# Kernel optimization log

Hardware: AMD Instinct MI355X
Metric: run time of the kernel (lower is better)

The kernel has to match this reference:

```python
import jax, jax.numpy as jnp
import numpy as np

N_STATE = 256   # complex state size n (real state is 2n)
N_IN = 128
BATCH = 16
T_STEPS = 2048
H_STEP = 0.01
EPS = 1e-3
LAM_RE_MIN, LAM_RE_MAX, MAX_PHASE = -5.0, -0.5, 6.283


def setup_inputs() -> dict:
    rng = np.random.default_rng(0)
    n, nu = N_STATE, N_IN
    # trainable params (as in torch __init__)
    u1 = rng.random(n)
    u2 = rng.random(n) * 2.0 - 1.0
    alpha = np.log(-(u1 * (LAM_RE_MAX - LAM_RE_MIN) + LAM_RE_MIN)).astype(np.float32)
    theta = (MAX_PHASE * u2).astype(np.float32)
    B_re = (rng.standard_normal((n, nu)) / np.sqrt(2.0 * nu)).astype(np.float32)
    B_im = (rng.standard_normal((n, nu)) / np.sqrt(2.0 * nu)).astype(np.float32)
    # fixed basis-change buffers: rho (normalized), T_inv, P = rho @ T_inv, Pinv
    H1 = rng.standard_normal((n, n))
    H2 = rng.standard_normal((n, n))
    rho = np.block([[H1, -H2], [H2, H1]])
    rho = rho / np.linalg.norm(rho)
    I = np.eye(n)
    T_inv = (1.0 / np.sqrt(2.0)) * np.block([[I, I], [-1j * I, 1j * I]])
    P = rho.astype(np.complex128) @ T_inv
    Pinv = np.linalg.inv(P)
    key = jax.random.key(0)
    k1, k2 = jax.random.split(key)
    return {
        "xi_init": jax.random.normal(k1, (BATCH, 1, 2 * n), dtype=jnp.float32),
        "u_log": jax.random.normal(k2, (BATCH, T_STEPS, nu), dtype=jnp.float32),
        "alpha": jnp.asarray(alpha),
        "theta": jnp.asarray(theta),
        "B_re": jnp.asarray(B_re),
        "B_im": jnp.asarray(B_im),
        "P_re": jnp.asarray(P.real, dtype=jnp.float32),
        "P_im": jnp.asarray(P.imag, dtype=jnp.float32),
        "Pinv_re": jnp.asarray(Pinv.real, dtype=jnp.float32),
        "Pinv_im": jnp.asarray(Pinv.imag, dtype=jnp.float32),
        "T": T_STEPS,
    }


def reference(xi_init, u_log, alpha, theta, B_re, B_im, P_re, P_im, Pinv_re, Pinv_im, T):
    n = alpha.shape[0]
    lam = (-jnp.exp(alpha) - EPS) + 1j * theta          # (n,) complex64
    Bc = B_re + 1j * B_im                               # (n, nu)
    P = P_re + 1j * P_im                                # (2n, 2n)
    Pinv = Pinv_re + 1j * Pinv_im                       # (2n, 2n)
    xi0 = xi_init[:, 0, :]                              # (B, 2n) real

    def step(xi, u_t):
        # xi: (B, 2n) real state; u_t: (B, nu)
        x_tilde = xi.astype(jnp.complex64) @ Pinv.T     # (B, 2n) complex
        x_bar = x_tilde[:, :n]                          # (B, n)
        x_bar_dot = lam * x_bar + u_t.astype(jnp.complex64) @ Bc.T
        x_tilde_dot = jnp.concatenate([x_bar_dot, jnp.conj(x_bar_dot)], axis=-1)
        x_dot = (x_tilde_dot @ P.T).real                # (B, 2n)
        xi_new = xi + H_STEP * x_dot
        return xi_new, xi_new

    u_seq = jnp.swapaxes(u_log, 0, 1)                   # (T, B, nu)
    _, xs = jax.lax.scan(step, xi0, u_seq)              # (T, B, 2n)
    # torch _sim logs xi_init, then skips xi after t=0, logs xi after t=1..T-1
    x_log = jnp.concatenate([xi0[None], xs[1:]], axis=0)  # (T, B, 2n)
    return jnp.swapaxes(x_log, 0, 1)                    # (B, T, 2n)
```

## Files before the change

kernel.cpp:

```cpp
#include <hip/hip_runtime.h>
#include <hip/hip_bf16.h>
#include <cstddef>
#include <cstdint>

#define N_ST 256
#define TWO_N 512
#define NU 128
#define BATCH 16
#define TSTEPS 2048
#define MTOT (BATCH * TSTEPS)
#define H_STEP 0.01f
#define EPS_V 0.001f
#define NCHUNK 32
#define CHUNKL 64

typedef __attribute__((ext_vector_type(4))) float f32x4;
typedef __attribute__((ext_vector_type(4))) short s16x4;
typedef __attribute__((ext_vector_type(8))) short s16x8;

#define OFF_FPK    0
#define OFF_ZPK    8388608
#define OFF_UPK    16777216
#define OFF_WT     18874368
#define OFF_WF     19005440
#define OFF_D      19038208
#define OFF_XBAR0  19039232
#define OFF_E      19047424
#define OFF_CINIT  19309568

static __device__ __forceinline__ float bf2f(short s) {
    return __uint_as_float(((unsigned)(unsigned short)s) << 16);
}

__global__ __launch_bounds__(256) void prep_all(
    const float* __restrict__ P_re, const float* __restrict__ P_im,
    const float* __restrict__ B_re, const float* __restrict__ B_im,
    const float* __restrict__ alpha, const float* __restrict__ theta,
    short* __restrict__ Wtpk, short* __restrict__ Wfpk,
    float* __restrict__ dbuf)
{
    int blk = blockIdx.x, tid = threadIdx.x;
    if (blk < 1024) {
        int idx = blk * 256 + tid;
        int j = idx >> 9, c = idx & 511;
        float v;
        if (c < N_ST) v = P_re[j * TWO_N + c] + P_re[j * TWO_N + c + N_ST];
        else          v = P_im[j * TWO_N + c] - P_im[j * TWO_N + c - N_ST];
        __hip_bfloat16 b = __float2bfloat16(v);
        Wtpk[((size_t)(j >> 4) * TWO_N + c) * 16 + (j & 15)] = *(short*)&b;
    } else if (blk < 1280) {
        int idx = (blk - 1024) * 256 + tid;
        int k = idx >> 9, c = idx & 511;
        float v = (c < N_ST) ? B_re[c * NU + k] : B_im[(c - N_ST) * NU + k];
        __hip_bfloat16 b = __float2bfloat16(H_STEP * v);
        Wfpk[((size_t)(c >> 4) * NU + k) * 16 + (c & 15)] = *(short*)&b;
    } else {
        int i = tid;
        float dr = 1.0f + H_STEP * (-expf(alpha[i]) - EPS_V);
        float di = H_STEP * theta[i];
        float pr = 1.0f, pi = 0.0f;
        for (int k = 0; k < CHUNKL; ++k) { float nr = pr * dr - pi * di; pi = pr * di + pi * dr; pr = nr; }
        dbuf[i] = dr; dbuf[N_ST + i] = di; dbuf[2 * N_ST + i] = pr; dbuf[3 * N_ST + i] = pi;
    }
}

__global__ __launch_bounds__(256) void xbar0_kernel(
    const float* __restrict__ Pinv_re, const float* __restrict__ Pinv_im,
    const float* __restrict__ xi0, float* __restrict__ xbar0)
{
    __shared__ float xs[BATCH * TWO_N];
    int tid = threadIdx.x;
#pragma unroll
    for (int q = 0; q < 8; ++q)
        *reinterpret_cast<float4*>(&xs[(q * 256 + tid) * 4]) =
            *reinterpret_cast<const float4*>(&xi0[(q * 256 + tid) * 4]);
    __syncthreads();

    int wv = tid >> 6, l = tid & 63;
    int i = blockIdx.x * 4 + wv;
    float rp[BATCH] = {}, ip[BATCH] = {};
#pragma unroll
    for (int q = 0; q < 8; ++q) {
        int j = q * 64 + l;
        float pr = Pinv_re[(size_t)i * TWO_N + j];
        float pi = Pinv_im[(size_t)i * TWO_N + j];
#pragma unroll
        for (int b = 0; b < BATCH; ++b) {
            float x = xs[b * TWO_N + j];
            rp[b] = fmaf(pr, x, rp[b]);
            ip[b] = fmaf(pi, x, ip[b]);
        }
    }
#pragma unroll
    for (int m = 1; m < 64; m <<= 1) {
#pragma unroll
        for (int b = 0; b < BATCH; ++b) {
            rp[b] += __shfl_xor(rp[b], m, 64);
            ip[b] += __shfl_xor(ip[b], m, 64);
        }
    }
    if (l == 0) {
#pragma unroll
        for (int b = 0; b < BATCH; ++b) {
            xbar0[b * TWO_N + i] = rp[b];
            xbar0[b * TWO_N + N_ST + i] = ip[b];
        }
    }
}

__global__ __launch_bounds__(256) void upack(const float* __restrict__ u, short* __restrict__ upk) {
    __shared__ short st[64 * 132];
    int tid = threadIdx.x, bid = blockIdx.x;
    const float* up = u + (size_t)bid * 8192;
#pragma unroll
    for (int q = 0; q < 8; ++q) {
        int idx = q * 1024 + tid * 4;
        float4 v = *reinterpret_cast<const float4*>(up + idx);
        int m = idx >> 7, k = idx & 127;
        s16x4 pv;
        __hip_bfloat16 b0 = __float2bfloat16(v.x); pv[0] = *(short*)&b0;
        __hip_bfloat16 b1 = __float2bfloat16(v.y); pv[1] = *(short*)&b1;
        __hip_bfloat16 b2 = __float2bfloat16(v.z); pv[2] = *(short*)&b2;
        __hip_bfloat16 b3 = __float2bfloat16(v.w); pv[3] = *(short*)&b3;
        *reinterpret_cast<__shared__ s16x4*>(&st[m * 132 + k]) = pv;
    }
    __syncthreads();
    short* op = upk + (size_t)bid * 8192;
#pragma unroll
    for (int q2 = 0; q2 < 4; ++q2) {
        int o = q2 * 2048 + tid * 8;
        int ml = o & 15, k = (o >> 4) & 127, sl = o >> 11;
        s16x8 w;
#pragma unroll
        for (int r = 0; r < 8; ++r) w[r] = st[(sl * 16 + ml + r) * 132 + k];
        *reinterpret_cast<s16x8*>(op + o) = w;
    }
}

template <int K, bool PACKOUT>
__global__ __launch_bounds__(256, 2) void gemm_mfma(const short* __restrict__ Apk,
                                                    const short* __restrict__ Bpk,
                                                    float* __restrict__ Cf,
                                                    short* __restrict__ Cp,
                                                    const float* __restrict__ xi0) {
    __shared__ __align__(1024) short lds[16384];
    const int tid = threadIdx.x;
    const int wid = tid >> 6, lane = tid & 63;
    const int m0 = blockIdx.x * 128, n0 = blockIdx.y * 128;
    const int wm = wid >> 1, wn = wid & 1;
    f32x4 acc[4][4] = {};
    const size_t slabStride = (size_t)K * 16;
    const unsigned ldsBase = (unsigned)(uintptr_t)(__attribute__((address_space(3))) short*)&lds[0];

#define STAGE(buf, kk)                                                                              \
    do {                                                                                            \
        const short* gA0 = Apk + ((size_t)(m0 >> 4) + wid)     * slabStride + (size_t)(kk) * 16 + lane * 8; \
        const short* gA1 = Apk + ((size_t)(m0 >> 4) + wid + 4) * slabStride + (size_t)(kk) * 16 + lane * 8; \
        const short* gB0 = Bpk + ((size_t)(n0 >> 4) + wid)     * slabStride + (size_t)(kk) * 16 + lane * 8; \
        const short* gB1 = Bpk + ((size_t)(n0 >> 4) + wid + 4) * slabStride + (size_t)(kk) * 16 + lane * 8; \
        __builtin_amdgcn_global_load_lds((const __attribute__((address_space(1))) void*)gA0,        \
            (__attribute__((address_space(3))) void*)&lds[(buf) * 4096 + wid * 512], 16, 0, 0);     \
        __builtin_amdgcn_global_load_lds((const __attribute__((address_space(1))) void*)gA1,        \
            (__attribute__((address_space(3))) void*)&lds[(buf) * 4096 + (wid + 4) * 512], 16, 0, 0); \
        __builtin_amdgcn_global_load_lds((const __attribute__((address_space(1))) void*)gB0,        \
            (__attribute__((address_space(3))) void*)&lds[8192 + (buf) * 4096 + wid * 512], 16, 0, 0); \
        __builtin_amdgcn_global_load_lds((const __attribute__((address_space(1))) void*)gB1,        \
            (__attribute__((address_space(3))) void*)&lds[8192 + (buf) * 4096 + (wid + 4) * 512], 16, 0, 0); \
    } while (0)

    STAGE(0, 0);
    asm volatile("s_waitcnt vmcnt(0)" ::: "memory");
    __syncthreads();
    int cur = 0;
    for (int kk = 0; kk < K; kk += 32) {
        if (kk + 32 < K) STAGE(cur ^ 1, kk + 32);

        s16x4 al[4], ah[4], bl[4], bh[4];
        const unsigned aB = ldsBase + (unsigned)cur * 8192;
        const unsigned bB = ldsBase + 16384u + (unsigned)cur * 8192;
#pragma unroll
        for (int t = 0; t < 4; ++t) {
            unsigned ad = aB + ((unsigned)(wm * 4 + t) << 10) + ((unsigned)lane << 3);
            unsigned bd = bB + ((unsigned)(wn * 4 + t) << 10) + ((unsigned)lane << 3);
            asm volatile("ds_read_b64_tr_b16 %0, %1 offset:0"   : "=v"(al[t]) : "v"(ad));
            asm volatile("ds_read_b64_tr_b16 %0, %1 offset:512" : "=v"(ah[t]) : "v"(ad));
            asm volatile("ds_read_b64_tr_b16 %0, %1 offset:0"   : "=v"(bl[t]) : "v"(bd));
            asm volatile("ds_read_b64_tr_b16 %0, %1 offset:512" : "=v"(bh[t]) : "v"(bd));
        }
        asm volatile("s_waitcnt lgkmcnt(0)" ::: "memory");
        __builtin_amdgcn_sched_barrier(0);

#pragma unroll
        for (int i = 0; i < 4; ++i) {
            s16x8 av = __builtin_shufflevector(al[i], ah[i], 0, 1, 2, 3, 4, 5, 6, 7);
#pragma unroll
            for (int j = 0; j < 4; ++j) {
                s16x8 bv = __builtin_shufflevector(bl[j], bh[j], 0, 1, 2, 3, 4, 5, 6, 7);
                acc[i][j] = __builtin_amdgcn_mfma_f32_16x16x32_bf16(av, bv, acc[i][j], 0, 0, 0);
            }
        }
        asm volatile("s_waitcnt vmcnt(0)" ::: "memory");
        __syncthreads();
        cur ^= 1;
    }
#undef STAGE

    const int cn = lane & 15;
    const int g4 = (lane >> 4) * 4;
    if (!PACKOUT) {
#pragma unroll
        for (int i = 0; i < 4; ++i) {
            int mrow = m0 + (wm * 4 + i) * 16 + g4;
#pragma unroll
            for (int j = 0; j < 4; ++j) {
                int ncol = n0 + (wn * 4 + j) * 16 + cn;
                float* cp = Cf + (size_t)mrow * TWO_N + ncol;
#pragma unroll
                for (int r = 0; r < 4; ++r) {
                    float v = acc[i][j][r];
                    if (((mrow + r) & (TSTEPS - 1)) == 0)
                        v = xi0[((mrow + r) >> 11) * TWO_N + ncol];
                    cp[(size_t)r * TWO_N] = v;
                }
            }
        }
    } else {
#pragma unroll
        for (int i = 0; i < 4; ++i) {
            int s = wm * 4 + i;
#pragma unroll
            for (int j = 0; j < 4; ++j) {
                int cwt = wn * 64 + j * 16 + cn;
                s16x4 pv;
#pragma unroll
                for (int r = 0; r < 4; ++r) {
                    __hip_bfloat16 bb = __float2bfloat16(acc[i][j][r]);
                    pv[r] = *reinterpret_cast<short*>(&bb);
                }
                *reinterpret_cast<__shared__ s16x4*>(&lds[((s * 128 + cwt) << 4) + g4]) = pv;
            }
        }
        __syncthreads();
        size_t baseG = (size_t)(m0 >> 4) * ((size_t)TWO_N * 16) + (size_t)n0 * 16;
#pragma unroll
        for (int q = 0; q < 8; ++q) {
            *reinterpret_cast<s16x8*>(Cp + baseG + (size_t)q * (TWO_N * 16) + tid * 8) =
                *reinterpret_cast<const __shared__ s16x8*>(&lds[q * 2048 + tid * 8]);
        }
    }
}

__global__ __launch_bounds__(256) void scan_passA(const short* __restrict__ Fpk,
                                                  const float* __restrict__ dbuf,
                                                  float* __restrict__ e) {
    int b = blockIdx.x, c = blockIdx.y, i = threadIdx.x;
    float dr = dbuf[i], di = dbuf[N_ST + i];
    float re = 0.f, im = 0.f;
    int slab0 = (b * TSTEPS + c * CHUNKL) >> 4;
#pragma unroll
    for (int g = 0; g < 4; ++g) {
        const short* base = Fpk + (size_t)(slab0 + g) * 8192 + i * 16;
        s16x8 r0 = *reinterpret_cast<const s16x8*>(base);
        s16x8 r1 = *reinterpret_cast<const s16x8*>(base + 8);
        s16x8 i0 = *reinterpret_cast<const s16x8*>(base + 4096);
        s16x8 i1 = *reinterpret_cast<const s16x8*>(base + 4096 + 8);
#pragma unroll
        for (int j = 0; j < 16; ++j) {
            float fr = bf2f(j < 8 ? r0[j & 7] : r1[j & 7]);
            float fi = bf2f(j < 8 ? i0[j & 7] : i1[j & 7]);
            float nre = fmaf(dr, re, fmaf(-di, im, fr));
            float nim = fmaf(dr, im, fmaf(di, re, fi));
            re = nre; im = nim;
        }
    }
    size_t o = ((size_t)(b * NCHUNK + c)) * TWO_N;
    e[o + i] = re;
    e[o + N_ST + i] = im;
}

__global__ void scan_passB(const float* __restrict__ e, const float* __restrict__ dbuf,
                           const float* __restrict__ xbar0, float* __restrict__ cinit) {
    int b = blockIdx.x, i = threadIdx.x;
    float dLr = dbuf[2 * N_ST + i], dLi = dbuf[3 * N_ST + i];
    float re = xbar0[b * TWO_N + i], im = xbar0[b * TWO_N + N_ST + i];
    for (int c = 0; c < NCHUNK; ++c) {
        size_t o = ((size_t)(b * NCHUNK + c)) * TWO_N;
        cinit[o + i] = re;
        cinit[o + N_ST + i] = im;
        float er = e[o + i], ei = e[o + N_ST + i];
        float nre = dLr * re - dLi * im + er;
        float nim = dLr * im + dLi * re + ei;
        re = nre; im = nim;
    }
}

__global__ __launch_bounds__(256) void scan_passC(const short* __restrict__ Fpk,
                                                  const float* __restrict__ dbuf,
                                                  const float* __restrict__ cinit,
                                                  short* __restrict__ Zpk) {
    int b = blockIdx.x, c = blockIdx.y, i = threadIdx.x;
    float dr = dbuf[i], di = dbuf[N_ST + i];
    size_t o = ((size_t)(b * NCHUNK + c)) * TWO_N;
    float re = cinit[o + i], im = cinit[o + N_ST + i];
    int slab0 = (b * TSTEPS + c * CHUNKL) >> 4;
#pragma unroll
    for (int g = 0; g < 4; ++g) {
        const short* base = Fpk + (size_t)(slab0 + g) * 8192 + i * 16;
        s16x8 r0 = *reinterpret_cast<const s16x8*>(base);
        s16x8 r1 = *reinterpret_cast<const s16x8*>(base + 8);
        s16x8 i0 = *reinterpret_cast<const s16x8*>(base + 4096);
        s16x8 i1 = *reinterpret_cast<const s16x8*>(base + 4096 + 8);
        s16x8 zr0, zr1, zi0, zi1;
#pragma unroll
        for (int j = 0; j < 16; ++j) {
            float fr = bf2f(j < 8 ? r0[j & 7] : r1[j & 7]);
            float fi = bf2f(j < 8 ? i0[j & 7] : i1[j & 7]);
            float nre = fmaf(dr, re, fmaf(-di, im, fr));
            float nim = fmaf(dr, im, fmaf(di, re, fi));
            re = nre; im = nim;
            __hip_bfloat16 br = __float2bfloat16(re), bi = __float2bfloat16(im);
            if (j < 8) { zr0[j & 7] = *(short*)&br; zi0[j & 7] = *(short*)&bi; }
            else       { zr1[j & 7] = *(short*)&br; zi1[j & 7] = *(short*)&bi; }
        }
        short* zb = Zpk + (size_t)(slab0 + g) * 8192 + i * 16;
        *reinterpret_cast<s16x8*>(zb)            = zr0;
        *reinterpret_cast<s16x8*>(zb + 8)        = zr1;
        *reinterpret_cast<s16x8*>(zb + 4096)     = zi0;
        *reinterpret_cast<s16x8*>(zb + 4096 + 8) = zi1;
    }
}

extern "C" void kernel_launch(void* const* d_in, const int* in_sizes, int n_in,
                              void* d_out, int out_size, void* d_ws, size_t ws_size,
                              hipStream_t stream) {
    const float* xi_init = (const float*)d_in[0];
    const float* u_log   = (const float*)d_in[1];
    const float* alpha   = (const float*)d_in[2];
    const float* theta   = (const float*)d_in[3];
    const float* B_re    = (const float*)d_in[4];
    const float* B_im    = (const float*)d_in[5];
    const float* P_re    = (const float*)d_in[6];
    const float* P_im    = (const float*)d_in[7];
    const float* Pinv_re = (const float*)d_in[8];
    const float* Pinv_im = (const float*)d_in[9];
    float* out = (float*)d_out;
    float* ws  = (float*)d_ws;

    short* Fpk  = (short*)(ws + OFF_FPK);
    short* Zpk  = (short*)(ws + OFF_ZPK);
    short* upk  = (short*)(ws + OFF_UPK);
    short* Wtpk = (short*)(ws + OFF_WT);
    short* Wfpk = (short*)(ws + OFF_WF);
    float* dbuf  = ws + OFF_D;
    float* xbar0 = ws + OFF_XBAR0;
    float* e     = ws + OFF_E;
    float* cinit = ws + OFF_CINIT;

    prep_all<<<1281, 256, 0, stream>>>(P_re, P_im, B_re, B_im, alpha, theta,
                                       Wtpk, Wfpk, dbuf);
    xbar0_kernel<<<64, 256, 0, stream>>>(Pinv_re, Pinv_im, xi_init, xbar0);
    upack<<<MTOT / 64, 256, 0, stream>>>(u_log, upk);

    gemm_mfma<NU, true><<<dim3(MTOT / 128, 4), 256, 0, stream>>>(
        upk, Wfpk, nullptr, Fpk, nullptr);

    scan_passA<<<dim3(BATCH, NCHUNK), 256, 0, stream>>>(Fpk, dbuf, e);
    scan_passB<<<BATCH, 256, 0, stream>>>(e, dbuf, xbar0, cinit);
    scan_passC<<<dim3(BATCH, NCHUNK), 256, 0, stream>>>(Fpk, dbuf, cinit, Zpk);

    gemm_mfma<TWO_N, false><<<dim3(MTOT / 128, 4), 256, 0, stream>>>(
        Zpk, Wtpk, out, nullptr, xi_init);
}
```

Baseline: 80.91 us.

## Triple-buffer GEMM LDS pipeline and fold chunk-carry scan into passC

The GEMM moves from double to triple buffering of LDS tiles. It keeps two stages in flight using partial vmcnt waits, adds a barrier after the LDS reads, and raises the occupancy hint to three blocks per CU. The serial scan_passB kernel is removed. Each scan_passC block now recomputes its own chunk-initial state by folding the preceding chunk carries, which saves a launch and a global round trip. The cost is redundant O(NCHUNK) work in later chunks and more LDS per GEMM block.

```diff
diff --git a/kernel.cpp b/kernel.cpp
--- a/kernel.cpp
+++ b/kernel.cpp
@@ -26,7 +26,6 @@
 #define OFF_D      19038208
 #define OFF_XBAR0  19039232
 #define OFF_E      19047424
-#define OFF_CINIT  19309568
 
 static __device__ __forceinline__ float bf2f(short s) {
     return __uint_as_float(((unsigned)(unsigned short)s) << 16);
@@ -138,12 +137,12 @@
 }
 
 template <int K, bool PACKOUT>
-__global__ __launch_bounds__(256, 2) void gemm_mfma(const short* __restrict__ Apk,
+__global__ __launch_bounds__(256, 3) void gemm_mfma(const short* __restrict__ Apk,
                                                     const short* __restrict__ Bpk,
                                                     float* __restrict__ Cf,
                                                     short* __restrict__ Cp,
                                                     const float* __restrict__ xi0) {
-    __shared__ __align__(1024) short lds[16384];
+    __shared__ __align__(1024) short lds[24576];
     const int tid = threadIdx.x;
     const int wid = tid >> 6, lane = tid & 63;
     const int m0 = blockIdx.x * 128, n0 = blockIdx.y * 128;
@@ -151,6 +150,7 @@
     f32x4 acc[4][4] = {};
     const size_t slabStride = (size_t)K * 16;
     const unsigned ldsBase = (unsigned)(uintptr_t)(__attribute__((address_space(3))) short*)&lds[0];
+    constexpr int NT = K / 32;
 
 #define STAGE(buf, kk)                                                                              \
     do {                                                                                            \
@@ -163,32 +163,39 @@
         __builtin_amdgcn_global_load_lds((const __attribute__((address_space(1))) void*)gA1,        \
             (__attribute__((address_space(3))) void*)&lds[(buf) * 4096 + (wid + 4) * 512], 16, 0, 0); \
         __builtin_amdgcn_global_load_lds((const __attribute__((address_space(1))) void*)gB0,        \
-            (__attribute__((address_space(3))) void*)&lds[8192 + (buf) * 4096 + wid * 512], 16, 0, 0); \
+            (__attribute__((address_space(3))) void*)&lds[12288 + (buf) * 4096 + wid * 512], 16, 0, 0); \
         __builtin_amdgcn_global_load_lds((const __attribute__((address_space(1))) void*)gB1,        \
-            (__attribute__((address_space(3))) void*)&lds[8192 + (buf) * 4096 + (wid + 4) * 512], 16, 0, 0); \
+            (__attribute__((address_space(3))) void*)&lds[12288 + (buf) * 4096 + (wid + 4) * 512], 16, 0, 0); \
     } while (0)
 
     STAGE(0, 0);
-    asm volatile("s_waitcnt vmcnt(0)" ::: "memory");
-    __syncthreads();
-    int cur = 0;
-    for (int kk = 0; kk < K; kk += 32) {
-        if (kk + 32 < K) STAGE(cur ^ 1, kk + 32);
+    STAGE(1, 32);
+
+#pragma unroll
+    for (int t = 0; t < NT; ++t) {
+        const int cur = t % 3;
+        if (t + 2 < NT) STAGE((t + 2) % 3, (t + 2) * 32);
+
+        if (t + 2 < NT)      asm volatile("s_waitcnt vmcnt(8)" ::: "memory");
+        else if (t + 1 < NT) asm volatile("s_waitcnt vmcnt(4)" ::: "memory");
+        else                 asm volatile("s_waitcnt vmcnt(0)" ::: "memory");
+        __syncthreads();
 
         s16x4 al[4], ah[4], bl[4], bh[4];
         const unsigned aB = ldsBase + (unsigned)cur * 8192;
-        const unsigned bB = ldsBase + 16384u + (unsigned)cur * 8192;
-#pragma unroll
-        for (int t = 0; t < 4; ++t) {
-            unsigned ad = aB + ((unsigned)(wm * 4 + t) << 10) + ((unsigned)lane << 3);
-            unsigned bd = bB + ((unsigned)(wn * 4 + t) << 10) + ((unsigned)lane << 3);
-            asm volatile("ds_read_b64_tr_b16 %0, %1 offset:0"   : "=v"(al[t]) : "v"(ad));
-            asm volatile("ds_read_b64_tr_b16 %0, %1 offset:512" : "=v"(ah[t]) : "v"(ad));
-            asm volatile("ds_read_b64_tr_b16 %0, %1 offset:0"   : "=v"(bl[t]) : "v"(bd));
-            asm volatile("ds_read_b64_tr_b16 %0, %1 offset:512" : "=v"(bh[t]) : "v"(bd));
+        const unsigned bB = ldsBase + 24576u + (unsigned)cur * 8192;
+#pragma unroll
+        for (int q = 0; q < 4; ++q) {
+            unsigned ad = aB + ((unsigned)(wm * 4 + q) << 10) + ((unsigned)lane << 3);
+            unsigned bd = bB + ((unsigned)(wn * 4 + q) << 10) + ((unsigned)lane << 3);
+            asm volatile("ds_read_b64_tr_b16 %0, %1 offset:0"   : "=v"(al[q]) : "v"(ad));
+            asm volatile("ds_read_b64_tr_b16 %0, %1 offset:512" : "=v"(ah[q]) : "v"(ad));
+            asm volatile("ds_read_b64_tr_b16 %0, %1 offset:0"   : "=v"(bl[q]) : "v"(bd));
+            asm volatile("ds_read_b64_tr_b16 %0, %1 offset:512" : "=v"(bh[q]) : "v"(bd));
         }
         asm volatile("s_waitcnt lgkmcnt(0)" ::: "memory");
         __builtin_amdgcn_sched_barrier(0);
+        __syncthreads();
 
 #pragma unroll
         for (int i = 0; i < 4; ++i) {
@@ -199,9 +206,6 @@
                 acc[i][j] = __builtin_amdgcn_mfma_f32_16x16x32_bf16(av, bv, acc[i][j], 0, 0, 0);
             }
         }
-        asm volatile("s_waitcnt vmcnt(0)" ::: "memory");
-        __syncthreads();
-        cur ^= 1;
     }
 #undef STAGE
 
@@ -225,6 +229,7 @@
             }
         }
     } else {
+        __syncthreads();
 #pragma unroll
         for (int i = 0; i < 4; ++i) {
             int s = wm * 4 + i;
@@ -278,30 +283,22 @@
     e[o + N_ST + i] = im;
 }
 
-__global__ void scan_passB(const float* __restrict__ e, const float* __restrict__ dbuf,
-                           const float* __restrict__ xbar0, float* __restrict__ cinit) {
-    int b = blockIdx.x, i = threadIdx.x;
-    float dLr = dbuf[2 * N_ST + i], dLi = dbuf[3 * N_ST + i];
-    float re = xbar0[b * TWO_N + i], im = xbar0[b * TWO_N + N_ST + i];
-    for (int c = 0; c < NCHUNK; ++c) {
-        size_t o = ((size_t)(b * NCHUNK + c)) * TWO_N;
-        cinit[o + i] = re;
-        cinit[o + N_ST + i] = im;
-        float er = e[o + i], ei = e[o + N_ST + i];
-        float nre = dLr * re - dLi * im + er;
-        float nim = dLr * im + dLi * re + ei;
-        re = nre; im = nim;
-    }
-}
-
 __global__ __launch_bounds__(256) void scan_passC(const short* __restrict__ Fpk,
                                                   const float* __restrict__ dbuf,
-                                                  const float* __restrict__ cinit,
+                                                  const float* __restrict__ e,
+                                                  const float* __restrict__ xbar0,
                                                   short* __restrict__ Zpk) {
     int b = blockIdx.x, c = blockIdx.y, i = threadIdx.x;
     float dr = dbuf[i], di = dbuf[N_ST + i];
-    size_t o = ((size_t)(b * NCHUNK + c)) * TWO_N;
-    float re = cinit[o + i], im = cinit[o + N_ST + i];
+    float dLr = dbuf[2 * N_ST + i], dLi = dbuf[3 * N_ST + i];
+    float re = xbar0[b * TWO_N + i], im = xbar0[b * TWO_N + N_ST + i];
+    for (int cc = 0; cc < c; ++cc) {
+        size_t o = ((size_t)(b * NCHUNK + cc)) * TWO_N;
+        float er = e[o + i], ei = e[o + N_ST + i];
+        float nre = fmaf(dLr, re, fmaf(-dLi, im, er));
+        float nim = fmaf(dLr, im, fmaf(dLi, re, ei));
+        re = nre; im = nim;
+    }
     int slab0 = (b * TSTEPS + c * CHUNKL) >> 4;
 #pragma unroll
     for (int g = 0; g < 4; ++g) {
@@ -354,7 +351,6 @@
     float* dbuf  = ws + OFF_D;
     float* xbar0 = ws + OFF_XBAR0;
     float* e     = ws + OFF_E;
-    float* cinit = ws + OFF_CINIT;
 
     prep_all<<<1281, 256, 0, stream>>>(P_re, P_im, B_re, B_im, alpha, theta,
                                        Wtpk, Wfpk, dbuf);
@@ -365,8 +361,7 @@
         upk, Wfpk, nullptr, Fpk, nullptr);
 
     scan_passA<<<dim3(BATCH, NCHUNK), 256, 0, stream>>>(Fpk, dbuf, e);
-    scan_passB<<<BATCH, 256, 0, stream>>>(e, dbuf, xbar0, cinit);
-    scan_passC<<<dim3(BATCH, NCHUNK), 256, 0, stream>>>(Fpk, dbuf, cinit, Zpk);
+    scan_passC<<<dim3(BATCH, NCHUNK), 256, 0, stream>>>(Fpk, dbuf, e, xbar0, Zpk);
 
     gemm_mfma<TWO_N, false><<<dim3(MTOT / 128, 4), 256, 0, stream>>>(
         Zpk, Wtpk, out, nullptr, xi_init);
```

Result: slower. 87.61 us (+8.3%).
